# Performance work log

Measured on AMD Instinct MI355X. Metric: run time of the kernel, lower is better.

## Reference

```python
import jax, jax.numpy as jnp
import numpy as np

B, T_IN, FEAT, UNITS, OUT_STEPS = 2048, 48, 64, 1024, 64


def setup_inputs() -> dict:
    key = jax.random.key(0)
    k0, k1, k2, k3 = jax.random.split(key, 4)
    inputs = jax.random.normal(k0, (B, T_IN, FEAT), dtype=jnp.float32)
    # glorot-ish scaling so gates don't saturate immediately
    W = jax.random.normal(k1, (FEAT, 4 * UNITS), dtype=jnp.float32) / np.sqrt(FEAT)
    U = jax.random.normal(k2, (UNITS, 4 * UNITS), dtype=jnp.float32) / np.sqrt(UNITS)
    b = jnp.zeros((4 * UNITS,), dtype=jnp.float32)
    Wd = jax.random.normal(k3, (UNITS, FEAT), dtype=jnp.float32) / np.sqrt(UNITS)
    bd = jnp.zeros((FEAT,), dtype=jnp.float32)
    return {"inputs": inputs, "W": W, "U": U, "b": b, "Wd": Wd, "bd": bd}


def _lstm_cell(h, c, x, W, U, b):
    # Keras LSTMCell gate order: i, f, g(candidate), o
    z = x @ W + h @ U + b  # [B, 4*units]
    i, f, g, o = jnp.split(z, 4, axis=-1)
    c = jax.nn.sigmoid(f) * c + jax.nn.sigmoid(i) * jnp.tanh(g)
    h = jax.nn.sigmoid(o) * jnp.tanh(c)
    return h, c


def reference(inputs, W, U, b, Wd, bd):
    batch = inputs.shape[0]
    units = U.shape[0]
    h0 = jnp.zeros((batch, units), dtype=inputs.dtype)
    c0 = jnp.zeros((batch, units), dtype=inputs.dtype)

    # warmup: run LSTM over the input sequence (time-major scan)
    def warm_step(carry, x_t):
        h, c = carry
        h, c = _lstm_cell(h, c, x_t, W, U, b)
        return (h, c), None

    (h, c), _ = jax.lax.scan(warm_step, (h0, c0), jnp.swapaxes(inputs, 0, 1))
    pred = h @ Wd + bd  # first prediction, [B, feat]

    def dec_step(carry, _):
        h, c, p = carry
        h, c = _lstm_cell(h, c, p, W, U, b)
        p = h @ Wd + bd
        return (h, c, p), p

    _, preds = jax.lax.scan(dec_step, (h, c, pred), None, length=OUT_STEPS - 1)
    preds = jnp.concatenate([pred[None], preds], axis=0)  # [out_steps, B, feat]
    return jnp.swapaxes(preds, 0, 1)  # [B, out_steps, feat]
```

## Files before the change

### kernel.cpp

```cpp
#include <hip/hip_runtime.h>
#include <hip/hip_bf16.h>

typedef float f32x4 __attribute__((ext_vector_type(4)));
typedef __bf16 bf16x8 __attribute__((ext_vector_type(8)));

#define B_SZ 2048
#define T_IN 48
#define FEAT 64
#define UNITS 1024
#define GCOLS 4096
#define OUT_STEPS 64
#define KWARM 1088

__device__ __forceinline__ int oc_of(int c) {
    return (((c >> 4) & 3) * UNITS) + ((c >> 6) * 16) + (c & 15);
}

typedef __attribute__((address_space(1))) const void gas_t;
typedef __attribute__((address_space(3))) void las_t;

__device__ __forceinline__ void gl_lds16(const void* g, void* l) {
    __builtin_amdgcn_global_load_lds((gas_t*)g, (las_t*)l, 16, 0, 0);
}
__device__ __forceinline__ float sigm(float x) {
    return __builtin_amdgcn_rcpf(1.0f + __expf(-x));
}
__device__ __forceinline__ float tanh_fast(float x) {
    float e = __expf(2.0f * x);
    return 1.0f - 2.0f * __builtin_amdgcn_rcpf(e + 1.0f);
}


__global__ __launch_bounds__(256) void reorder_UW(const float* __restrict__ U, const float* __restrict__ W,
                                                  __hip_bfloat16* __restrict__ UTw) {
    __shared__ __hip_bfloat16 t[64][64];
    const int k0 = blockIdx.x * 64;
    const int c0 = blockIdx.y * 64;
    const int tid = threadIdx.x;
#pragma unroll
    for (int i = 0; i < 16; ++i) {
        int idx = tid + i * 256;
        int rk = idx >> 6, cc = idx & 63;
        int k = k0 + rk, c = c0 + cc;
        int oc = oc_of(c);
        float v = (k < UNITS) ? U[(size_t)k * GCOLS + oc] : W[(size_t)(k - UNITS) * GCOLS + oc];
        t[rk][cc] = __float2bfloat16(v);
    }
    __syncthreads();
#pragma unroll
    for (int i = 0; i < 16; ++i) {
        int idx = tid + i * 256;
        int rc = idx >> 6, kk = idx & 63;
        UTw[(size_t)(c0 + rc) * KWARM + k0 + kk] = t[kk][rc];
    }
}

__global__ __launch_bounds__(256) void transpose_Wd(const float* __restrict__ Wd, __hip_bfloat16* __restrict__ WdT) {
    __shared__ __hip_bfloat16 t[64][64];
    const int k0 = blockIdx.x * 64;
    const int tid = threadIdx.x;
#pragma unroll
    for (int i = 0; i < 16; ++i) {
        int idx = tid + i * 256;
        int rk = idx >> 6, ff = idx & 63;
        t[rk][ff] = __float2bfloat16(Wd[(size_t)(k0 + rk) * FEAT + ff]);
    }
    __syncthreads();
#pragma unroll
    for (int i = 0; i < 16; ++i) {
        int idx = tid + i * 256;
        int rf = idx >> 6, kk = idx & 63;
        WdT[(size_t)rf * UNITS + k0 + kk] = t[kk][rf];
    }
}

__global__ __launch_bounds__(256) void build_UTdec(const __hip_bfloat16* __restrict__ UTw,
                                                   const __hip_bfloat16* __restrict__ WdT,
                                                   __hip_bfloat16* __restrict__ UTd) {
    __shared__ float Wl[64][16];
    const int k = blockIdx.x * 256 + threadIdx.x;
    const int c0 = blockIdx.y * 16;
    const int tid = threadIdx.x;
#pragma unroll
    for (int i = 0; i < 4; ++i) {
        int idx = tid + i * 256;
        int f = idx >> 4, cc = idx & 15;
        Wl[f][cc] = __bfloat162float(UTw[(size_t)(c0 + cc) * KWARM + UNITS + f]);
    }
    __syncthreads();
    float acc[16];
#pragma unroll
    for (int cc = 0; cc < 16; ++cc) acc[cc] = 0.f;
    for (int f = 0; f < 64; ++f) {
        float wd = __bfloat162float(WdT[(size_t)f * UNITS + k]);
#pragma unroll
        for (int cc = 0; cc < 16; ++cc) acc[cc] += wd * Wl[f][cc];
    }
#pragma unroll
    for (int cc = 0; cc < 16; ++cc) {
        float uv = __bfloat162float(UTw[(size_t)(c0 + cc) * KWARM + k]);
        UTd[(size_t)(c0 + cc) * UNITS + k] = __float2bfloat16(uv + acc[cc]);
    }
}

__global__ __launch_bounds__(256) void build_bias(const float* __restrict__ b, const float* __restrict__ bd,
                                                  const __hip_bfloat16* __restrict__ UTw,
                                                  float* __restrict__ bw, float* __restrict__ bdc) {
    const int c = blockIdx.x * 256 + threadIdx.x;
    const int oc = oc_of(c);
    float base = b[oc];
    float s = 0.f;
    for (int f = 0; f < FEAT; ++f) s += bd[f] * __bfloat162float(UTw[(size_t)c * KWARM + UNITS + f]);
    bw[c] = base;
    bdc[c] = base + s;
}

__global__ void convert_x(const float* __restrict__ x, __hip_bfloat16* __restrict__ xb, int n) {
    int i = blockIdx.x * blockDim.x + threadIdx.x;
    if (i < n) xb[i] = __float2bfloat16(x[i]);
}

template <bool WARM, bool PRED>
__global__ __launch_bounds__(256) void lstm_step(
    const __hip_bfloat16* __restrict__ hin,
    const __hip_bfloat16* __restrict__ xbf, int t,
    const __hip_bfloat16* __restrict__ UT,
    const float* __restrict__ bias,
    float* __restrict__ cst,
    __hip_bfloat16* __restrict__ hout,
    const __hip_bfloat16* __restrict__ WdT,
    const float* __restrict__ bd,
    float* __restrict__ out, int tstep)
{
    constexpr int KD = WARM ? KWARM : UNITS;
    constexpr int NKT = KD / 64;

    __shared__ alignas(16) __hip_bfloat16 Al[2 * 8192];
    __shared__ alignas(16) __hip_bfloat16 Bl[2 * 8192];
    __shared__ alignas(16) __hip_bfloat16 Wl[PRED ? 2 * 4096 : 8];

    const int tid = threadIdx.x;
    const int lane = tid & 63;
    const int wv = tid >> 6;
    const int wr = wv >> 1, wc = wv & 1;
    const int bid = blockIdx.x;
    const int xcd = bid & 7;
    const int i6 = bid >> 3;
    const int mb = xcd * 2 + (i6 & 1);
    const int nb = i6 >> 1;
    const int m0 = mb * 128;
    const int n0 = nb * 128;
    const bool doPred = PRED && (nb == 0);

    f32x4 acc[4][4] = {};
    f32x4 accp[2][4] = {};

    const int lrow = lane >> 3;
    const int scol = ((lane & 7) * 16) ^ (lrow << 4);

    const char* aS[4]; const char* bS[4]; const char* xS[4]; const char* wS[2];
#pragma unroll
    for (int r = 0; r < 4; ++r) {
        int row = (r * 4 + wv) * 8 + lrow;
        aS[r] = (const char*)hin + (size_t)(m0 + row) * (UNITS * 2) + scol;
        bS[r] = (const char*)UT + (size_t)(n0 + row) * (KD * 2) + scol;
        if (WARM) xS[r] = (const char*)xbf + (size_t)(m0 + row) * (T_IN * FEAT * 2) + (size_t)t * (FEAT * 2) + scol;
    }
    if (PRED && doPred) {
#pragma unroll
        for (int r = 0; r < 2; ++r) {
            int row = (r * 4 + wv) * 8 + lrow;
            wS[r] = (const char*)WdT + (size_t)row * (UNITS * 2) + scol;
        }
    }

    const int u16 = lane & 15;
    const int unit = (nb * 2 + wc) * 16 + u16;
    const int rbase = m0 + 64 * wr + ((lane >> 4) << 2);
    float bv[4];
#pragma unroll
    for (int g = 0; g < 4; ++g) bv[g] = bias[n0 + 64 * wc + 16 * g + u16];
    float bdv[4];
    if (PRED && doPred) {
#pragma unroll
        for (int ni = 0; ni < 4; ++ni) bdv[ni] = bd[16 * ni + u16];
    }

    auto stage = [&](int kt) {
        const int buf = kt & 1;
#pragma unroll
        for (int r = 0; r < 4; ++r) {
            const char* s = (WARM && kt == NKT - 1) ? xS[r] : (aS[r] + kt * 128);
            gl_lds16(s, (char*)Al + buf * 16384 + (r * 4 + wv) * 1024);
        }
#pragma unroll
        for (int r = 0; r < 4; ++r)
            gl_lds16(bS[r] + kt * 128, (char*)Bl + buf * 16384 + (r * 4 + wv) * 1024);
        if (PRED && doPred) {
#pragma unroll
            for (int r = 0; r < 2; ++r)
                gl_lds16(wS[r] + kt * 128, (char*)Wl + buf * 8192 + (r * 4 + wv) * 1024);
        }
    };

    const int ar = lane & 15;
    const int ko = (lane >> 4) << 3;
    const int swz = (ar & 7) << 3;

    auto compute = [&](int kt) {
        const int buf = kt & 1;
#pragma unroll
        for (int kk = 0; kk < 2; ++kk) {
            bf16x8 af[4], bfr[4];
#pragma unroll
            for (int mi = 0; mi < 4; ++mi)
                af[mi] = *reinterpret_cast<const bf16x8*>(&Al[buf * 8192 + (64 * wr + 16 * mi + ar) * 64 + ((32 * kk + ko) ^ swz)]);
#pragma unroll
            for (int ni = 0; ni < 4; ++ni)
                bfr[ni] = *reinterpret_cast<const bf16x8*>(&Bl[buf * 8192 + (64 * wc + 16 * ni + ar) * 64 + ((32 * kk + ko) ^ swz)]);
#pragma unroll
            for (int mi = 0; mi < 4; ++mi)
#pragma unroll
                for (int ni = 0; ni < 4; ++ni)
                    acc[mi][ni] = __builtin_amdgcn_mfma_f32_16x16x32_bf16(af[mi], bfr[ni], acc[mi][ni], 0, 0, 0);
            if (PRED && doPred) {
#pragma unroll
                for (int ni = 0; ni < 4; ++ni) {
                    bf16x8 bp = *reinterpret_cast<const bf16x8*>(&Wl[buf * 4096 + (16 * ni + ar) * 64 + ((32 * kk + ko) ^ swz)]);
#pragma unroll
                    for (int pi = 0; pi < 2; ++pi)
                        accp[pi][ni] = __builtin_amdgcn_mfma_f32_16x16x32_bf16(af[2 * wc + pi], bp, accp[pi][ni], 0, 0, 0);
                }
            }
        }
    };

    stage(0);
#pragma unroll
    for (int kt = 0; kt < NKT - 1; ++kt) {
        stage(kt + 1);
        if (PRED && doPred) asm volatile("s_waitcnt vmcnt(10) lgkmcnt(0)" ::: "memory");
        else                asm volatile("s_waitcnt vmcnt(8) lgkmcnt(0)" ::: "memory");
        __builtin_amdgcn_s_barrier();
        compute(kt);
        __builtin_amdgcn_s_barrier();
    }
    float cv[16];
#pragma unroll
    for (int mi = 0; mi < 4; ++mi)
#pragma unroll
        for (int reg = 0; reg < 4; ++reg)
            cv[mi * 4 + reg] = cst[(size_t)(rbase + 16 * mi + reg) * UNITS + unit];
    asm volatile("s_waitcnt vmcnt(16) lgkmcnt(0)" ::: "memory");
    __builtin_amdgcn_s_barrier();
    compute(NKT - 1);

#pragma unroll
    for (int mi = 0; mi < 4; ++mi)
#pragma unroll
        for (int reg = 0; reg < 4; ++reg) {
            float zi = acc[mi][0][reg] + bv[0];
            float zf = acc[mi][1][reg] + bv[1];
            float zg = acc[mi][2][reg] + bv[2];
            float zo = acc[mi][3][reg] + bv[3];
            float cn = sigm(zf) * cv[mi * 4 + reg] + sigm(zi) * tanh_fast(zg);
            size_t idx = (size_t)(rbase + 16 * mi + reg) * UNITS + unit;
            cst[idx] = cn;
            hout[idx] = __float2bfloat16(sigm(zo) * tanh_fast(cn));
        }

    if (PRED && doPred) {
#pragma unroll
        for (int ni = 0; ni < 4; ++ni) {
#pragma unroll
            for (int pi = 0; pi < 2; ++pi) {
                const int prow = m0 + 64 * wr + 32 * wc + 16 * pi + ((lane >> 4) << 2);
                f32x4 v = accp[pi][ni];
#pragma unroll
                for (int reg = 0; reg < 4; ++reg)
                    out[(size_t)(prow + reg) * (OUT_STEPS * FEAT) + (size_t)tstep * FEAT + (16 * ni + u16)] = v[reg] + bdv[ni];
            }
        }
    }
}

extern "C" void kernel_launch(void* const* d_in, const int* in_sizes, int n_in,
                              void* d_out, int out_size, void* d_ws, size_t ws_size,
                              hipStream_t stream) {
    const float* inputs = (const float*)d_in[0];
    const float* W  = (const float*)d_in[1];
    const float* U  = (const float*)d_in[2];
    const float* b  = (const float*)d_in[3];
    const float* Wd = (const float*)d_in[4];
    const float* bd = (const float*)d_in[5];
    float* out = (float*)d_out;

    char* ws = (char*)d_ws;
    size_t off = 0;
    auto alloc = [&](size_t bytes) { char* p = ws + off; off = (off + bytes + 255) & ~255ULL; return p; };
    __hip_bfloat16* UTw = (__hip_bfloat16*)alloc((size_t)GCOLS * KWARM * 2);
    __hip_bfloat16* UTd = (__hip_bfloat16*)alloc((size_t)GCOLS * UNITS * 2);
    __hip_bfloat16* WdT = (__hip_bfloat16*)alloc((size_t)FEAT * UNITS * 2);
    __hip_bfloat16* Xbf = (__hip_bfloat16*)alloc((size_t)B_SZ * T_IN * FEAT * 2);
    __hip_bfloat16* hA  = (__hip_bfloat16*)alloc((size_t)B_SZ * UNITS * 2);
    __hip_bfloat16* hB  = (__hip_bfloat16*)alloc((size_t)B_SZ * UNITS * 2);
    float* cst = (float*)alloc((size_t)B_SZ * UNITS * 4);
    float* bw  = (float*)alloc(GCOLS * 4);
    float* bdc = (float*)alloc(GCOLS * 4);

    hipMemsetAsync(cst, 0, (size_t)B_SZ * UNITS * 4, stream);
    hipMemsetAsync(hA, 0, (size_t)B_SZ * UNITS * 2, stream);

    dim3 blk(256);
    reorder_UW<<<dim3(17, 64), blk, 0, stream>>>(U, W, UTw);
    transpose_Wd<<<dim3(16), blk, 0, stream>>>(Wd, WdT);
    build_UTdec<<<dim3(4, 256), blk, 0, stream>>>(UTw, WdT, UTd);
    build_bias<<<dim3(16), blk, 0, stream>>>(b, bd, UTw, bw, bdc);
    {
        int n = B_SZ * T_IN * FEAT;
        convert_x<<<dim3((n + 255) / 256), blk, 0, stream>>>(inputs, Xbf, n);
    }

    const __hip_bfloat16* cur = hA;
    __hip_bfloat16* nxt = hB;
    for (int t = 0; t < T_IN; ++t) {
        lstm_step<true, false><<<dim3(512), blk, 0, stream>>>(cur, Xbf, t, UTw, bw, cst, nxt,
                                                              nullptr, nullptr, nullptr, 0);
        __hip_bfloat16* tmp = (__hip_bfloat16*)cur; cur = nxt; nxt = tmp;
    }
    for (int t = 1; t <= OUT_STEPS; ++t) {
        lstm_step<false, true><<<dim3(512), blk, 0, stream>>>(cur, nullptr, 0, UTd, bdc, cst, nxt,
                                                              WdT, bd, out, t - 1);
        __hip_bfloat16* tmp = (__hip_bfloat16*)cur; cur = nxt; nxt = tmp;
    }
}
```

Measured before the change: 5.170 ms.

## Load U tiles directly into registers, remap blocks, and spread prediction across blocks

New measurement: 8.283 ms. 60.2% more time.

```diff
diff --git a/kernel.cpp b/kernel.cpp
--- a/kernel.cpp
+++ b/kernel.cpp
@@ -121,7 +121,7 @@
 }
 
 template <bool WARM, bool PRED>
-__global__ __launch_bounds__(256) void lstm_step(
+__global__ __launch_bounds__(256, 3) void lstm_step(
     const __hip_bfloat16* __restrict__ hin,
     const __hip_bfloat16* __restrict__ xbf, int t,
     const __hip_bfloat16* __restrict__ UT,
@@ -136,43 +136,45 @@
     constexpr int NKT = KD / 64;
 
     __shared__ alignas(16) __hip_bfloat16 Al[2 * 8192];
-    __shared__ alignas(16) __hip_bfloat16 Bl[2 * 8192];
-    __shared__ alignas(16) __hip_bfloat16 Wl[PRED ? 2 * 4096 : 8];
 
     const int tid = threadIdx.x;
     const int lane = tid & 63;
     const int wv = tid >> 6;
     const int wr = wv >> 1, wc = wv & 1;
     const int bid = blockIdx.x;
-    const int xcd = bid & 7;
-    const int i6 = bid >> 3;
-    const int mb = xcd * 2 + (i6 & 1);
-    const int nb = i6 >> 1;
+    const int x = bid & 7;
+    const int bl = bid >> 3;
+    const int mb = ((x >> 2) << 3) + (bl >> 3);
+    const int nb = ((x & 3) << 3) + (bl & 7);
     const int m0 = mb * 128;
     const int n0 = nb * 128;
-    const bool doPred = PRED && (nb == 0);
+    const bool doPred = PRED && (nb < 4);
 
     f32x4 acc[4][4] = {};
-    f32x4 accp[2][4] = {};
+    f32x4 accp[2] = {};
 
     const int lrow = lane >> 3;
     const int scol = ((lane & 7) * 16) ^ (lrow << 4);
 
-    const char* aS[4]; const char* bS[4]; const char* xS[4]; const char* wS[2];
+    const char* aS[4]; const char* xS[4];
 #pragma unroll
     for (int r = 0; r < 4; ++r) {
         int row = (r * 4 + wv) * 8 + lrow;
         aS[r] = (const char*)hin + (size_t)(m0 + row) * (UNITS * 2) + scol;
-        bS[r] = (const char*)UT + (size_t)(n0 + row) * (KD * 2) + scol;
         if (WARM) xS[r] = (const char*)xbf + (size_t)(m0 + row) * (T_IN * FEAT * 2) + (size_t)t * (FEAT * 2) + scol;
     }
-    if (PRED && doPred) {
-#pragma unroll
-        for (int r = 0; r < 2; ++r) {
-            int row = (r * 4 + wv) * 8 + lrow;
-            wS[r] = (const char*)WdT + (size_t)row * (UNITS * 2) + scol;
-        }
-    }
+
+    const int ar = lane & 15;
+    const int ko = (lane >> 4) << 3;
+    const int swz = (ar & 7) << 3;
+
+    const char* bB[4];
+#pragma unroll
+    for (int ni = 0; ni < 4; ++ni)
+        bB[ni] = (const char*)UT + ((size_t)(n0 + 64 * wc + 16 * ni + ar) * KD + ko) * 2;
+    const char* wB = nullptr;
+    if (PRED && doPred)
+        wB = (const char*)WdT + ((size_t)(16 * nb + ar) * UNITS + ko) * 2;
 
     const int u16 = lane & 15;
     const int unit = (nb * 2 + wc) * 16 + u16;
@@ -180,69 +182,63 @@
     float bv[4];
 #pragma unroll
     for (int g = 0; g < 4; ++g) bv[g] = bias[n0 + 64 * wc + 16 * g + u16];
-    float bdv[4];
-    if (PRED && doPred) {
-#pragma unroll
-        for (int ni = 0; ni < 4; ++ni) bdv[ni] = bd[16 * ni + u16];
-    }
-
-    auto stage = [&](int kt) {
+    float bdv = 0.f;
+    if (PRED && doPred) bdv = bd[16 * nb + u16];
+
+    auto stageA = [&](int kt) {
         const int buf = kt & 1;
 #pragma unroll
         for (int r = 0; r < 4; ++r) {
             const char* s = (WARM && kt == NKT - 1) ? xS[r] : (aS[r] + kt * 128);
             gl_lds16(s, (char*)Al + buf * 16384 + (r * 4 + wv) * 1024);
         }
-#pragma unroll
-        for (int r = 0; r < 4; ++r)
-            gl_lds16(bS[r] + kt * 128, (char*)Bl + buf * 16384 + (r * 4 + wv) * 1024);
+    };
+
+    bf16x8 Bf[8];
+    bf16x8 Wf[2];
+    auto loadB = [&](int kt) {
+#pragma unroll
+        for (int kk = 0; kk < 2; ++kk)
+#pragma unroll
+            for (int ni = 0; ni < 4; ++ni)
+                Bf[kk * 4 + ni] = *reinterpret_cast<const bf16x8*>(bB[ni] + kt * 128 + kk * 64);
         if (PRED && doPred) {
 #pragma unroll
-            for (int r = 0; r < 2; ++r)
-                gl_lds16(wS[r] + kt * 128, (char*)Wl + buf * 8192 + (r * 4 + wv) * 1024);
+            for (int kk = 0; kk < 2; ++kk)
+                Wf[kk] = *reinterpret_cast<const bf16x8*>(wB + kt * 128 + kk * 64);
         }
     };
-
-    const int ar = lane & 15;
-    const int ko = (lane >> 4) << 3;
-    const int swz = (ar & 7) << 3;
 
     auto compute = [&](int kt) {
         const int buf = kt & 1;
 #pragma unroll
         for (int kk = 0; kk < 2; ++kk) {
-            bf16x8 af[4], bfr[4];
+            bf16x8 af[4];
 #pragma unroll
             for (int mi = 0; mi < 4; ++mi)
                 af[mi] = *reinterpret_cast<const bf16x8*>(&Al[buf * 8192 + (64 * wr + 16 * mi + ar) * 64 + ((32 * kk + ko) ^ swz)]);
 #pragma unroll
-            for (int ni = 0; ni < 4; ++ni)
-                bfr[ni] = *reinterpret_cast<const bf16x8*>(&Bl[buf * 8192 + (64 * wc + 16 * ni + ar) * 64 + ((32 * kk + ko) ^ swz)]);
-#pragma unroll
             for (int mi = 0; mi < 4; ++mi)
 #pragma unroll
                 for (int ni = 0; ni < 4; ++ni)
-                    acc[mi][ni] = __builtin_amdgcn_mfma_f32_16x16x32_bf16(af[mi], bfr[ni], acc[mi][ni], 0, 0, 0);
+                    acc[mi][ni] = __builtin_amdgcn_mfma_f32_16x16x32_bf16(af[mi], Bf[kk * 4 + ni], acc[mi][ni], 0, 0, 0);
             if (PRED && doPred) {
 #pragma unroll
-                for (int ni = 0; ni < 4; ++ni) {
-                    bf16x8 bp = *reinterpret_cast<const bf16x8*>(&Wl[buf * 4096 + (16 * ni + ar) * 64 + ((32 * kk + ko) ^ swz)]);
-#pragma unroll
-                    for (int pi = 0; pi < 2; ++pi)
-                        accp[pi][ni] = __builtin_amdgcn_mfma_f32_16x16x32_bf16(af[2 * wc + pi], bp, accp[pi][ni], 0, 0, 0);
-                }
+                for (int pi = 0; pi < 2; ++pi)
+                    accp[pi] = __builtin_amdgcn_mfma_f32_16x16x32_bf16(af[2 * wc + pi], Wf[kk], accp[pi], 0, 0, 0);
             }
         }
     };
 
-    stage(0);
+    stageA(0);
+    loadB(0);
 #pragma unroll
     for (int kt = 0; kt < NKT - 1; ++kt) {
-        stage(kt + 1);
-        if (PRED && doPred) asm volatile("s_waitcnt vmcnt(10) lgkmcnt(0)" ::: "memory");
-        else                asm volatile("s_waitcnt vmcnt(8) lgkmcnt(0)" ::: "memory");
+        stageA(kt + 1);
+        asm volatile("s_waitcnt vmcnt(4) lgkmcnt(0)" ::: "memory");
         __builtin_amdgcn_s_barrier();
         compute(kt);
+        loadB(kt + 1);
         __builtin_amdgcn_s_barrier();
     }
     float cv[16];
@@ -271,15 +267,12 @@
 
     if (PRED && doPred) {
 #pragma unroll
-        for (int ni = 0; ni < 4; ++ni) {
-#pragma unroll
-            for (int pi = 0; pi < 2; ++pi) {
-                const int prow = m0 + 64 * wr + 32 * wc + 16 * pi + ((lane >> 4) << 2);
-                f32x4 v = accp[pi][ni];
-#pragma unroll
-                for (int reg = 0; reg < 4; ++reg)
-                    out[(size_t)(prow + reg) * (OUT_STEPS * FEAT) + (size_t)tstep * FEAT + (16 * ni + u16)] = v[reg] + bdv[ni];
-            }
+        for (int pi = 0; pi < 2; ++pi) {
+            const int prow = m0 + 64 * wr + 32 * wc + 16 * pi + ((lane >> 4) << 2);
+            f32x4 v = accp[pi];
+#pragma unroll
+            for (int reg = 0; reg < 4; ++reg)
+                out[(size_t)(prow + reg) * (OUT_STEPS * FEAT) + (size_t)tstep * FEAT + (16 * nb + u16)] = v[reg] + bdv;
         }
     }
 }
```
